# Kernel optimization log

Measured on AMD Instinct MI355X. Metric: run time of the kernel, lower is better.

## Reference

```python
import math
import jax, jax.numpy as jnp
import numpy as np

D_MODEL = 128
MLCV_DIM = 2


def make_pe(N, d):
    """Faithful vectorization of PositionalEncodingMatrix (d divisible by 4)."""
    Q = d // 4
    ks = jnp.arange(0, d, 4, dtype=jnp.float32)          # [Q]
    i = jnp.arange(N, dtype=jnp.float32)[:, None, None]  # [N,1,1]
    j = jnp.arange(N, dtype=jnp.float32)[None, :, None]  # [1,N,1]
    rel = jnp.abs(i - j)                                  # [N,N,1]
    div0 = 10000.0 ** (ks / d)
    div2 = 10000.0 ** ((ks + 2.0) / d)
    div3 = 10000.0 ** ((ks + 3.0) / d)
    ch0 = jnp.broadcast_to(jnp.sin(i / div0), (N, N, Q))
    ch1 = jnp.broadcast_to(jnp.cos(i / div0), (N, N, Q))
    ch2 = jnp.broadcast_to(jnp.sin(j / div2), (N, N, Q))
    ch3 = jnp.cos(rel / div3)
    return jnp.stack([ch0, ch1, ch2, ch3], axis=-1).reshape(N, N, d)


def setup_inputs() -> dict:
    key = jax.random.key(0)
    ks = jax.random.split(key, 12)
    B, P, d = 128, 4950, D_MODEL
    s = lambda fan: 1.0 / math.sqrt(fan)
    return {
        "cad_distances": jax.random.uniform(ks[0], (B, P), dtype=jnp.float32) * 20.0,
        "w_dist": jax.random.normal(ks[1], (d,), dtype=jnp.float32) * s(1),
        "b_dist": jax.random.normal(ks[2], (d,), dtype=jnp.float32) * s(1),
        "w_enc1": jax.random.normal(ks[3], (d, d), dtype=jnp.float32) * s(d),
        "b_enc1": jnp.zeros((d,), jnp.float32),
        "w_enc2": jax.random.normal(ks[4], (d, d), dtype=jnp.float32) * s(d),
        "b_enc2": jnp.zeros((d,), jnp.float32),
        "w_out1": jax.random.normal(ks[5], (d, 64), dtype=jnp.float32) * s(d),
        "b_out1": jnp.zeros((64,), jnp.float32),
        "w_out2": jax.random.normal(ks[6], (64, MLCV_DIM), dtype=jnp.float32) * s(64),
        "b_out2": jnp.zeros((MLCV_DIM,), jnp.float32),
    }


def reference(cad_distances, w_dist, b_dist, w_enc1, b_enc1, w_enc2, b_enc2,
              w_out1, b_out1, w_out2, b_out2):
    B, P = cad_distances.shape
    d = w_dist.shape[0]
    N = int((1 + math.sqrt(1 + 8 * P)) / 2)
    iu0, iu1 = np.triu_indices(N, 1)  # matches nested-loop pair ordering

    # distance embedding: Linear(1, d)
    emb = cad_distances[:, :, None] * w_dist + b_dist        # [B,P,d]

    # mean over dim=2 of symmetric scatter == per-row sum of edge embeddings / N
    emb_t = emb.transpose(1, 0, 2)                           # [P,B,d]
    row = (jax.ops.segment_sum(emb_t, jnp.asarray(iu0), num_segments=N)
           + jax.ops.segment_sum(emb_t, jnp.asarray(iu1), num_segments=N))
    row = row.transpose(1, 0, 2)                             # [B,N,d]

    pe_row = make_pe(N, d).sum(axis=1)                       # [N,d]
    x1d = (row + pe_row[None]) / N                           # [B,N,d]

    # encoder MLP
    h = jax.nn.relu(jnp.einsum('bnd,de->bne', x1d, w_enc1) + b_enc1)
    h = jax.nn.relu(jnp.einsum('bnd,de->bne', h, w_enc2) + b_enc2)

    # AdaptiveAvgPool1d(1) over sequence dim
    pooled = h.mean(axis=1)                                  # [B,d]

    out = jax.nn.relu(pooled @ w_out1 + b_out1)
    return out @ w_out2 + b_out2                             # [B, mlcv_dim]
```

## Files before the change

kernel.cpp:

```cpp
#include <hip/hip_runtime.h>

#define NN 100
#define D  128
#define BB 128
#define PP 4950

#define U_OFF    0
#define V_OFF    (D)
#define S_OFF    (V_OFF + NN * D)
#define POOL_OFF (S_OFF + BB * NN)

__device__ inline void fma4(float4& a, float s, const float4& w) {
    a.x = fmaf(s, w.x, a.x);
    a.y = fmaf(s, w.y, a.y);
    a.z = fmaf(s, w.z, a.z);
    a.w = fmaf(s, w.w, a.w);
}

__global__ __launch_bounds__(256)
void prep_kernel(const float* __restrict__ cad,
                 const float* __restrict__ w_dist,
                 const float* __restrict__ b_dist,
                 const float* __restrict__ w1,
                 const float* __restrict__ b1,
                 float* __restrict__ ws) {
    const int blk = blockIdx.x;
    const int t   = threadIdx.x;

    if (blk < NN) {
        __shared__ float pe_l[D];
        const int n = blk;
        if (t < D) {
            const int c = t & 3;
            const int q = t >> 2;
            const float kf = (float)(4 * q);
            const float LOG1E4_OVER_D = 9.210340371976184f / 128.0f;
            float val;
            if (c == 0) {
                float inv = expf(-kf * LOG1E4_OVER_D);
                val = (float)NN * sinf((float)n * inv);
            } else if (c == 1) {
                float inv = expf(-kf * LOG1E4_OVER_D);
                val = (float)NN * cosf((float)n * inv);
            } else if (c == 2) {
                float inv = expf(-(kf + 2.0f) * LOG1E4_OVER_D);
                float s = 0.f;
                for (int j = 0; j < NN; ++j) s += sinf((float)j * inv);
                val = s;
            } else {
                float inv = expf(-(kf + 3.0f) * LOG1E4_OVER_D);
                float s = 0.f;
                for (int j = 0; j < NN; ++j) s += cosf(fabsf((float)(n - j)) * inv);
                val = s;
            }
            pe_l[t] = val;
        }
        __syncthreads();
        if (t < D) {
            float acc = 0.f;
            #pragma unroll 4
            for (int dd = 0; dd < D; ++dd) {
                float x = fmaf(99.0f, b_dist[dd], pe_l[dd]);
                acc = fmaf(x, w1[dd * D + t], acc);
            }
            ws[V_OFF + n * D + t] = acc * (1.0f / (float)NN) + b1[t];
        }
    } else if (blk == NN) {
        if (t < D) {
            float acc = 0.f;
            #pragma unroll 4
            for (int dd = 0; dd < D; ++dd) acc = fmaf(w_dist[dd], w1[dd * D + t], acc);
            ws[U_OFF + t] = acc;
        }
    } else if (blk == NN + 1) {
        float4 z = {0.f, 0.f, 0.f, 0.f};
        for (int i = t; i < BB * D / 4; i += 256)
            ((float4*)(ws + POOL_OFF))[i] = z;
    } else {
        const int b = blk - (NN + 2);
        __shared__ float S_l[NN];
        if (t < NN) S_l[t] = 0.f;
        __syncthreads();
        const float* cb = cad + b * PP;
        for (int p = t; p < PP; p += 256) {
            float val = cb[p];
            int i = (int)((199.0f - sqrtf((float)(39601 - 8 * p))) * 0.5f);
            while (i * (199 - i) / 2 > p) --i;
            while ((i + 1) * (198 - i) / 2 <= p) ++i;
            int j = p - i * (199 - i) / 2 + i + 1;
            atomicAdd(&S_l[i], val);
            atomicAdd(&S_l[j], val);
        }
        __syncthreads();
        if (t < NN) ws[S_OFF + b * NN + t] = S_l[t] * (1.0f / (float)NN);
    }
}

__global__ __launch_bounds__(256)
void gemm2_kernel(const float* __restrict__ w2,
                  const float* __restrict__ b2,
                  const float* __restrict__ ws) {
    const int chunk = blockIdx.x;
    const int b     = blockIdx.y;
    const int tid   = threadIdx.x;
    const int base  = chunk * 32;

    __shared__ float w2_l[D * D];
    __shared__ float h1_l[32 * D];

    const float* u_g = ws + U_OFF;
    const float* v_g = ws + V_OFF;
    const float* S_g = ws + S_OFF + b * NN;
    float*       pool_g = (float*)(ws + POOL_OFF) + b * D;

    for (int i = tid; i < D * D / 4; i += 256)
        ((float4*)w2_l)[i] = ((const float4*)w2)[i];

    {
        const int dd0 = (tid & 31) * 4;
        const int r0  = tid >> 5;
        const float4 uv = *(const float4*)(u_g + dd0);
        #pragma unroll
        for (int k = 0; k < 4; ++k) {
            const int lr = r0 + k * 8;
            const int g  = base + lr;
            float4 h = {0.f, 0.f, 0.f, 0.f};
            if (g < NN) {
                const float s = S_g[g];
                const float4 vv = *(const float4*)(v_g + g * D + dd0);
                h.x = fmaxf(fmaf(s, uv.x, vv.x), 0.f);
                h.y = fmaxf(fmaf(s, uv.y, vv.y), 0.f);
                h.z = fmaxf(fmaf(s, uv.z, vv.z), 0.f);
                h.w = fmaxf(fmaf(s, uv.w, vv.w), 0.f);
            }
            *(float4*)(h1_l + lr * D + dd0) = h;
        }
    }
    __syncthreads();

    const int eq   = tid & 31;
    const int slot = tid >> 5;
    const int e0   = eq * 4;
    const int lr0  = slot * 4;
    const int g0   = base + lr0;

    float4 pool = {0.f, 0.f, 0.f, 0.f};
    if (g0 < NN) {
        const float4 b2v = *(const float4*)(b2 + e0);
        float4 acc0 = {0,0,0,0}, acc1 = {0,0,0,0};
        float4 acc2 = {0,0,0,0}, acc3 = {0,0,0,0};
        #pragma unroll 2
        for (int dd = 0; dd < D; dd += 4) {
            const float4 w0  = *(const float4*)&w2_l[(dd + 0) * D + e0];
            const float4 w1v = *(const float4*)&w2_l[(dd + 1) * D + e0];
            const float4 w2v = *(const float4*)&w2_l[(dd + 2) * D + e0];
            const float4 w3v = *(const float4*)&w2_l[(dd + 3) * D + e0];
            float4 h;
            h = *(const float4*)&h1_l[(lr0 + 0) * D + dd];
            fma4(acc0, h.x, w0); fma4(acc0, h.y, w1v); fma4(acc0, h.z, w2v); fma4(acc0, h.w, w3v);
            h = *(const float4*)&h1_l[(lr0 + 1) * D + dd];
            fma4(acc1, h.x, w0); fma4(acc1, h.y, w1v); fma4(acc1, h.z, w2v); fma4(acc1, h.w, w3v);
            h = *(const float4*)&h1_l[(lr0 + 2) * D + dd];
            fma4(acc2, h.x, w0); fma4(acc2, h.y, w1v); fma4(acc2, h.z, w2v); fma4(acc2, h.w, w3v);
            h = *(const float4*)&h1_l[(lr0 + 3) * D + dd];
            fma4(acc3, h.x, w0); fma4(acc3, h.y, w1v); fma4(acc3, h.z, w2v); fma4(acc3, h.w, w3v);
        }
        if (g0 + 0 < NN) {
            pool.x += fmaxf(acc0.x + b2v.x, 0.f); pool.y += fmaxf(acc0.y + b2v.y, 0.f);
            pool.z += fmaxf(acc0.z + b2v.z, 0.f); pool.w += fmaxf(acc0.w + b2v.w, 0.f);
        }
        if (g0 + 1 < NN) {
            pool.x += fmaxf(acc1.x + b2v.x, 0.f); pool.y += fmaxf(acc1.y + b2v.y, 0.f);
            pool.z += fmaxf(acc1.z + b2v.z, 0.f); pool.w += fmaxf(acc1.w + b2v.w, 0.f);
        }
        if (g0 + 2 < NN) {
            pool.x += fmaxf(acc2.x + b2v.x, 0.f); pool.y += fmaxf(acc2.y + b2v.y, 0.f);
            pool.z += fmaxf(acc2.z + b2v.z, 0.f); pool.w += fmaxf(acc2.w + b2v.w, 0.f);
        }
        if (g0 + 3 < NN) {
            pool.x += fmaxf(acc3.x + b2v.x, 0.f); pool.y += fmaxf(acc3.y + b2v.y, 0.f);
            pool.z += fmaxf(acc3.z + b2v.z, 0.f); pool.w += fmaxf(acc3.w + b2v.w, 0.f);
        }
    }
    __syncthreads();

    *(float4*)(h1_l + slot * D + e0) = pool;
    __syncthreads();
    if (tid < D) {
        float s = 0.f;
        #pragma unroll
        for (int sl = 0; sl < 8; ++sl) s += h1_l[sl * D + tid];
        atomicAdd(&pool_g[tid], s);
    }
}

__global__ __launch_bounds__(64)
void head_kernel(const float* __restrict__ wo1,
                 const float* __restrict__ bo1,
                 const float* __restrict__ wo2,
                 const float* __restrict__ bo2,
                 const float* __restrict__ ws,
                 float* __restrict__ out) {
    const int b = blockIdx.x;
    const int t = threadIdx.x;
    __shared__ float z_l[64];

    const float* pooled = ws + POOL_OFF + b * D;
    float acc = bo1[t];
    #pragma unroll 4
    for (int e = 0; e < D; ++e)
        acc = fmaf(pooled[e] * (1.0f / (float)NN), wo1[e * 64 + t], acc);
    z_l[t] = fmaxf(acc, 0.f);
    __syncthreads();

    if (t < 2) {
        float o = bo2[t];
        #pragma unroll 4
        for (int k = 0; k < 64; ++k) o = fmaf(z_l[k], wo2[k * 2 + t], o);
        out[b * 2 + t] = o;
    }
}

extern "C" void kernel_launch(void* const* d_in, const int* in_sizes, int n_in,
                              void* d_out, int out_size, void* d_ws, size_t ws_size,
                              hipStream_t stream) {
    const float* cad    = (const float*)d_in[0];
    const float* w_dist = (const float*)d_in[1];
    const float* b_dist = (const float*)d_in[2];
    const float* w1     = (const float*)d_in[3];
    const float* b1     = (const float*)d_in[4];
    const float* w2     = (const float*)d_in[5];
    const float* b2     = (const float*)d_in[6];
    const float* wo1    = (const float*)d_in[7];
    const float* bo1    = (const float*)d_in[8];
    const float* wo2    = (const float*)d_in[9];
    const float* bo2    = (const float*)d_in[10];
    float* ws  = (float*)d_ws;
    float* out = (float*)d_out;

    prep_kernel<<<dim3(NN + 2 + BB), dim3(256), 0, stream>>>(cad, w_dist, b_dist, w1, b1, ws);
    gemm2_kernel<<<dim3(4, BB), dim3(256), 0, stream>>>(w2, b2, ws);
    head_kernel<<<dim3(BB), dim3(64), 0, stream>>>(wo1, bo1, wo2, bo2, ws, out);
}
```

Baseline: 128.5 us.

## Use closed-form PE sums and fuse head into gemm2 via last-block counter

Result: slower. 167.3 us (+30.2%).

```diff
diff --git a/kernel.cpp b/kernel.cpp
--- a/kernel.cpp
+++ b/kernel.cpp
@@ -9,6 +9,7 @@
 #define V_OFF    (D)
 #define S_OFF    (V_OFF + NN * D)
 #define POOL_OFF (S_OFF + BB * NN)
+#define CNT_OFF  (POOL_OFF + BB * D)
 
 __device__ inline void fma4(float4& a, float s, const float4& w) {
     a.x = fmaf(s, w.x, a.x);
@@ -27,57 +28,58 @@
     const int blk = blockIdx.x;
     const int t   = threadIdx.x;
 
-    if (blk < NN) {
-        __shared__ float pe_l[D];
-        const int n = blk;
-        if (t < D) {
-            const int c = t & 3;
-            const int q = t >> 2;
+    if (blk < NN / 2) {
+        __shared__ float pe_l[2][D];
+        const int half = t >> 7;
+        const int tl   = t & 127;
+        const int n    = 2 * blk + half;
+        {
+            const int c = tl & 3;
+            const int q = tl >> 2;
             const float kf = (float)(4 * q);
-            const float LOG1E4_OVER_D = 9.210340371976184f / 128.0f;
+            const float L = 9.210340371976184f / 128.0f;
             float val;
             if (c == 0) {
-                float inv = expf(-kf * LOG1E4_OVER_D);
-                val = (float)NN * sinf((float)n * inv);
+                float a = expf(-kf * L);
+                val = (float)NN * sinf((float)n * a);
             } else if (c == 1) {
-                float inv = expf(-kf * LOG1E4_OVER_D);
-                val = (float)NN * cosf((float)n * inv);
+                float a = expf(-kf * L);
+                val = (float)NN * cosf((float)n * a);
             } else if (c == 2) {
-                float inv = expf(-(kf + 2.0f) * LOG1E4_OVER_D);
-                float s = 0.f;
-                for (int j = 0; j < NN; ++j) s += sinf((float)j * inv);
-                val = s;
+                float a = expf(-(kf + 2.0f) * L);
+                val = sinf(50.0f * a) * sinf(49.5f * a) / sinf(0.5f * a);
             } else {
-                float inv = expf(-(kf + 3.0f) * LOG1E4_OVER_D);
-                float s = 0.f;
-                for (int j = 0; j < NN; ++j) s += cosf(fabsf((float)(n - j)) * inv);
-                val = s;
+                float a = expf(-(kf + 3.0f) * L);
+                val = (sinf(((float)n + 0.5f) * a) + sinf((99.5f - (float)n) * a))
+                      / (2.0f * sinf(0.5f * a));
             }
-            pe_l[t] = val;
-        }
-        __syncthreads();
+            pe_l[half][tl] = val;
+        }
+        __syncthreads();
+        {
+            float acc = 0.f;
+            #pragma unroll 4
+            for (int dd = 0; dd < D; ++dd) {
+                float x = fmaf(99.0f, b_dist[dd], pe_l[half][dd]);
+                acc = fmaf(x, w1[dd * D + tl], acc);
+            }
+            ws[V_OFF + n * D + tl] = acc * (1.0f / (float)NN) + b1[tl];
+        }
+    } else if (blk == NN / 2) {
         if (t < D) {
             float acc = 0.f;
             #pragma unroll 4
-            for (int dd = 0; dd < D; ++dd) {
-                float x = fmaf(99.0f, b_dist[dd], pe_l[dd]);
-                acc = fmaf(x, w1[dd * D + t], acc);
-            }
-            ws[V_OFF + n * D + t] = acc * (1.0f / (float)NN) + b1[t];
-        }
-    } else if (blk == NN) {
-        if (t < D) {
-            float acc = 0.f;
-            #pragma unroll 4
             for (int dd = 0; dd < D; ++dd) acc = fmaf(w_dist[dd], w1[dd * D + t], acc);
             ws[U_OFF + t] = acc;
-        }
-    } else if (blk == NN + 1) {
-        float4 z = {0.f, 0.f, 0.f, 0.f};
-        for (int i = t; i < BB * D / 4; i += 256)
-            ((float4*)(ws + POOL_OFF))[i] = z;
+        } else {
+            const int tl = t - 128;
+            float4 z = {0.f, 0.f, 0.f, 0.f};
+            for (int i = tl; i < BB * D / 4; i += 128)
+                ((float4*)(ws + POOL_OFF))[i] = z;
+            ((int*)(ws + CNT_OFF))[tl] = 0;
+        }
     } else {
-        const int b = blk - (NN + 2);
+        const int b = blk - (NN / 2 + 1);
         __shared__ float S_l[NN];
         if (t < NN) S_l[t] = 0.f;
         __syncthreads();
@@ -99,7 +101,12 @@
 __global__ __launch_bounds__(256)
 void gemm2_kernel(const float* __restrict__ w2,
                   const float* __restrict__ b2,
-                  const float* __restrict__ ws) {
+                  const float* __restrict__ wo1,
+                  const float* __restrict__ bo1,
+                  const float* __restrict__ wo2,
+                  const float* __restrict__ bo2,
+                  float* __restrict__ ws,
+                  float* __restrict__ out) {
     const int chunk = blockIdx.x;
     const int b     = blockIdx.y;
     const int tid   = threadIdx.x;
@@ -107,11 +114,13 @@
 
     __shared__ float w2_l[D * D];
     __shared__ float h1_l[32 * D];
-
-    const float* u_g = ws + U_OFF;
-    const float* v_g = ws + V_OFF;
-    const float* S_g = ws + S_OFF + b * NN;
-    float*       pool_g = (float*)(ws + POOL_OFF) + b * D;
+    __shared__ int   last_l;
+
+    const float* u_g    = ws + U_OFF;
+    const float* v_g    = ws + V_OFF;
+    const float* S_g    = ws + S_OFF + b * NN;
+    float*       pool_g = ws + POOL_OFF + b * D;
+    int*         cnt_g  = (int*)(ws + CNT_OFF);
 
     for (int i = tid; i < D * D / 4; i += 256)
         ((float4*)w2_l)[i] = ((const float4*)w2)[i];
@@ -192,32 +201,28 @@
         for (int sl = 0; sl < 8; ++sl) s += h1_l[sl * D + tid];
         atomicAdd(&pool_g[tid], s);
     }
-}
-
-__global__ __launch_bounds__(64)
-void head_kernel(const float* __restrict__ wo1,
-                 const float* __restrict__ bo1,
-                 const float* __restrict__ wo2,
-                 const float* __restrict__ bo2,
-                 const float* __restrict__ ws,
-                 float* __restrict__ out) {
-    const int b = blockIdx.x;
-    const int t = threadIdx.x;
-    __shared__ float z_l[64];
-
-    const float* pooled = ws + POOL_OFF + b * D;
-    float acc = bo1[t];
-    #pragma unroll 4
-    for (int e = 0; e < D; ++e)
-        acc = fmaf(pooled[e] * (1.0f / (float)NN), wo1[e * 64 + t], acc);
-    z_l[t] = fmaxf(acc, 0.f);
-    __syncthreads();
-
-    if (t < 2) {
-        float o = bo2[t];
-        #pragma unroll 4
-        for (int k = 0; k < 64; ++k) o = fmaf(z_l[k], wo2[k * 2 + t], o);
-        out[b * 2 + t] = o;
+    __threadfence();
+    __syncthreads();
+    if (tid == 0) last_l = (atomicAdd(&cnt_g[b], 1) == 3);
+    __syncthreads();
+
+    if (last_l) {
+        __threadfence();
+        if (tid < D) h1_l[tid] = pool_g[tid] * (1.0f / (float)NN);
+        __syncthreads();
+        if (tid < 64) {
+            float acc = bo1[tid];
+            #pragma unroll 4
+            for (int e = 0; e < D; ++e) acc = fmaf(h1_l[e], wo1[e * 64 + tid], acc);
+            h1_l[D + tid] = fmaxf(acc, 0.f);
+        }
+        __syncthreads();
+        if (tid < 2) {
+            float o = bo2[tid];
+            #pragma unroll 4
+            for (int k = 0; k < 64; ++k) o = fmaf(h1_l[D + k], wo2[k * 2 + tid], o);
+            out[b * 2 + tid] = o;
+        }
     }
 }
 
@@ -238,7 +243,6 @@
     float* ws  = (float*)d_ws;
     float* out = (float*)d_out;
 
-    prep_kernel<<<dim3(NN + 2 + BB), dim3(256), 0, stream>>>(cad, w_dist, b_dist, w1, b1, ws);
-    gemm2_kernel<<<dim3(4, BB), dim3(256), 0, stream>>>(w2, b2, ws);
-    head_kernel<<<dim3(BB), dim3(64), 0, stream>>>(wo1, bo1, wo2, bo2, ws, out);
-}
+    prep_kernel<<<dim3(NN / 2 + 1 + BB), dim3(256), 0, stream>>>(cad, w_dist, b_dist, w1, b1, ws);
+    gemm2_kernel<<<dim3(4, BB), dim3(256), 0, stream>>>(w2, b2, wo1, bo1, wo2, bo2, ws, out);
+}
```
